# Kernel tuning notes

Measured on AMD Instinct MI355X. Metric: run time of the kernel, lower is better.

## Reference

```python
import jax, jax.numpy as jnp
import numpy as np

N = 12500      # nodes
E = 200000     # edges (avg degree 16)
IN = 32        # inp_dim
OUT = 32       # out_dim
ATTN = 32      # attn_rel_emb_dim
R = 200        # num_rels
NB = 50        # num_bases


def setup_inputs() -> dict:
    key = jax.random.key(0)
    ks = jax.random.split(key, 10)
    node_feat = jax.random.normal(ks[0], (N, IN), jnp.float32)
    total_edge = jax.random.randint(ks[1], (2, E), 0, N)
    total_target_relation = jax.random.normal(ks[2], (E, ATTN), jnp.float32)
    total_relation_embed = jax.random.normal(ks[3], (E, ATTN), jnp.float32)
    total_relation = jax.random.randint(ks[4], (E,), 0, R)
    # learned parameters (xavier-ish scale)
    weight = jax.random.normal(ks[5], (NB, IN, OUT), jnp.float32) * 0.1
    w_comp = jax.random.normal(ks[6], (R, NB), jnp.float32) * 0.1
    self_loop_weight = jax.random.normal(ks[7], (IN, OUT), jnp.float32) * 0.1
    A_w = jax.random.normal(ks[8], (IN, 2 * IN + 2 * ATTN), jnp.float32) * 0.1
    A_b = jnp.zeros((IN,), jnp.float32)
    B_w = jax.random.normal(ks[9], (1, IN), jnp.float32) * 0.1
    B_b = jnp.zeros((1,), jnp.float32)
    return {
        'node_feat': node_feat,
        'total_target_relation': total_target_relation,
        'total_relation_embed': total_relation_embed,
        'weight': weight,
        'w_comp': w_comp,
        'self_loop_weight': self_loop_weight,
        'A_w': A_w,
        'A_b': A_b,
        'B_w': B_w,
        'B_b': B_b,
        'total_edge': total_edge,
        'total_relation': total_relation,
    }


def reference(node_feat, total_target_relation, total_relation_embed,
              weight, w_comp, self_loop_weight, A_w, A_b, B_w, B_b,
              total_edge, total_relation):
    # basis decomposition: per-relation weight [R, IN, OUT]
    rel_w = jnp.einsum('rb,bio->rio', w_comp, weight)
    src = node_feat[total_edge[0]]            # [E, IN]
    tgt = node_feat[total_edge[1]]            # [E, IN]
    # per-edge relation-specific transform (bmm in torch)
    msg = jnp.einsum('ei,eio->eo', src, rel_w[total_relation])  # [E, OUT]
    curr = tgt @ self_loop_weight             # [E, OUT]
    # attention MLP: sigmoid(B(relu(A(concat))))
    e = jnp.concatenate([src, tgt, total_relation_embed, total_target_relation], axis=1)
    h = jax.nn.relu(e @ A_w.T + A_b)
    a = jax.nn.sigmoid(h @ B_w.T + B_b)       # [E, 1]
    curr = curr + msg * a
    # gnn_spmm(e2n_sp, curr): scatter-add edge messages to target nodes
    out = jax.ops.segment_sum(curr, total_edge[1], num_segments=node_feat.shape[0])
    return out  # [N, OUT]
```

## Files before the change

kernel.cpp:

```cpp
#include <hip/hip_runtime.h>

#define N_NODES 12500
#define N_EDGES 200000
#define DIM 32
#define N_REL 200
#define N_BASES 50

#define OUT_ELEMS   (N_NODES * DIM)
#define ZERO_BLOCKS ((OUT_ELEMS + 1023) / 1024)

#define AWBF_OFF  (N_REL * 1024 * 2)
#define SLWT_OFF  (AWBF_OFF + 32 * 128 * 2)

typedef __attribute__((ext_vector_type(8))) short short8;
typedef __attribute__((ext_vector_type(4))) float f32x4;
typedef __attribute__((ext_vector_type(4))) unsigned short us4;

__device__ __forceinline__ unsigned short f2bf(float x) {
    union { float f; unsigned u; } v; v.f = x;
    unsigned r = (v.u + 0x7FFFu + ((v.u >> 16) & 1u)) >> 16;
    return (unsigned short)r;
}

__device__ __forceinline__ short8 cvt8(float4 a, float4 b) {
    short8 r;
    r[0] = (short)f2bf(a.x); r[1] = (short)f2bf(a.y);
    r[2] = (short)f2bf(a.z); r[3] = (short)f2bf(a.w);
    r[4] = (short)f2bf(b.x); r[5] = (short)f2bf(b.y);
    r[6] = (short)f2bf(b.z); r[7] = (short)f2bf(b.w);
    return r;
}

#define MFMA(A, B, C) __builtin_amdgcn_mfma_f32_16x16x32_bf16(A, B, C, 0, 0, 0)

__global__ __launch_bounds__(256) void prep_kernel(
    const float* __restrict__ weight,
    const float* __restrict__ w_comp,
    const float* __restrict__ Aw,
    const float* __restrict__ slw,
    unsigned short* __restrict__ relw_bf,
    unsigned short* __restrict__ aw_bf,
    unsigned short* __restrict__ slwT_bf,
    float* __restrict__ out)
{
    int b = blockIdx.x, tid = threadIdx.x;
    if (b < N_REL) {
        __shared__ float wc[N_BASES];
        if (tid < N_BASES) wc[tid] = w_comp[b * N_BASES + tid];
        __syncthreads();
        const float* wp = weight + tid * 4;
        float4 acc = make_float4(0.f, 0.f, 0.f, 0.f);
        #pragma unroll 10
        for (int bb = 0; bb < N_BASES; bb++) {
            float4 w = *(const float4*)(wp + bb * 1024);
            float c = wc[bb];
            acc.x = fmaf(c, w.x, acc.x); acc.y = fmaf(c, w.y, acc.y);
            acc.z = fmaf(c, w.z, acc.z); acc.w = fmaf(c, w.w, acc.w);
        }
        us4 o;
        o[0] = f2bf(acc.x); o[1] = f2bf(acc.y);
        o[2] = f2bf(acc.z); o[3] = f2bf(acc.w);
        *(us4*)(relw_bf + b * 1024 + tid * 4) = o;
    } else if (b < N_REL + ZERO_BLOCKS) {
        int base = (b - N_REL) * 1024 + tid * 4;
        if (base + 3 < OUT_ELEMS)
            *(float4*)(out + base) = make_float4(0.f, 0.f, 0.f, 0.f);
        else
            for (int k = 0; k < 4; k++)
                if (base + k < OUT_ELEMS) out[base + k] = 0.f;
    } else {
        for (int x = tid; x < 32 * 128; x += 256) aw_bf[x] = f2bf(Aw[x]);
        for (int x = tid; x < 32 * 32; x += 256) {
            int i = x >> 5, j = x & 31;
            slwT_bf[j * 32 + i] = f2bf(slw[x]);
        }
    }
}

__global__ __launch_bounds__(256) void edge_kernel(
    const float* __restrict__ node_feat,
    const float* __restrict__ ttr,
    const float* __restrict__ tre,
    const float* __restrict__ Ab,
    const float* __restrict__ Bw,
    const float* __restrict__ Bb,
    const int*  __restrict__ edge0,
    const int*  __restrict__ edge1,
    const int*  __restrict__ rel,
    const unsigned short* __restrict__ relw_bf,
    const unsigned short* __restrict__ aw_bf,
    const unsigned short* __restrict__ slwT_bf,
    float* __restrict__ out)
{
    __shared__ float msgL[4 * 16 * 36];

    int tid  = threadIdx.x;
    int wave = tid >> 6;
    int lane = tid & 63;
    int m = lane & 15;
    int q = lane >> 4;
    int base = blockIdx.x * 64 + wave * 16;

    int s_ld = 0, t_ld = 0, r_ld = 0;
    if (lane < 16) {
        int eid = base + lane;
        int s = edge0[eid]; s_ld = s < 0 ? 0 : (s >= N_NODES ? N_NODES - 1 : s);
        int t = edge1[eid]; t_ld = t < 0 ? 0 : (t >= N_NODES ? N_NODES - 1 : t);
        int r = rel[eid];   r_ld = r < 0 ? 0 : (r >= N_REL   ? N_REL   - 1 : r);
    }
    int s_m = __shfl(s_ld, m, 64);
    int t_m = __shfl(t_ld, m, 64);
    int eid_m = base + m;

    const float* sp = node_feat + s_m * DIM + q * 8;
    float4 sv0 = *(const float4*)sp, sv1 = *(const float4*)(sp + 4);
    const float* tp = node_feat + t_m * DIM + q * 8;
    float4 tv0 = *(const float4*)tp, tv1 = *(const float4*)(tp + 4);
    const float* rp = tre + eid_m * DIM + q * 8;
    float4 rv0 = *(const float4*)rp, rv1 = *(const float4*)(rp + 4);
    const float* qp = ttr + eid_m * DIM + q * 8;
    float4 qv0 = *(const float4*)qp, qv1 = *(const float4*)(qp + 4);

    short8 fsrc = cvt8(sv0, sv1);
    short8 ftgt = cvt8(tv0, tv1);
    short8 fre  = cvt8(rv0, rv1);
    short8 ftr  = cvt8(qv0, qv1);

    short8 bA[4][2], bS[2];
    #pragma unroll
    for (int hh = 0; hh < 2; hh++) {
        #pragma unroll
        for (int c = 0; c < 4; c++)
            bA[c][hh] = *(const short8*)(aw_bf + (16 * hh + m) * 128 + 32 * c + 8 * q);
        bS[hh] = *(const short8*)(slwT_bf + (16 * hh + m) * 32 + 8 * q);
    }

    float ab0 = Ab[m], ab1 = Ab[16 + m];
    f32x4 hacc0 = {ab0, ab0, ab0, ab0};
    f32x4 hacc1 = {ab1, ab1, ab1, ab1};
    f32x4 cacc0 = {0.f, 0.f, 0.f, 0.f};
    f32x4 cacc1 = {0.f, 0.f, 0.f, 0.f};

    hacc0 = MFMA(fsrc, bA[0][0], hacc0);  hacc1 = MFMA(fsrc, bA[0][1], hacc1);
    hacc0 = MFMA(ftgt, bA[1][0], hacc0);  hacc1 = MFMA(ftgt, bA[1][1], hacc1);
    hacc0 = MFMA(fre,  bA[2][0], hacc0);  hacc1 = MFMA(fre,  bA[2][1], hacc1);
    hacc0 = MFMA(ftr,  bA[3][0], hacc0);  hacc1 = MFMA(ftr,  bA[3][1], hacc1);
    cacc0 = MFMA(ftgt, bS[0], cacc0);     cacc1 = MFMA(ftgt, bS[1], cacc1);

    int e_loc = lane >> 2;
    int cq    = lane & 3;
    int r_e = __shfl(r_ld, e_loc, 64);
    const unsigned short* rwb = relw_bf + r_e * 1024 + cq * 8;
    float sf[8] = {sv0.x, sv0.y, sv0.z, sv0.w, sv1.x, sv1.y, sv1.z, sv1.w};
    float msg[8] = {0.f, 0.f, 0.f, 0.f, 0.f, 0.f, 0.f, 0.f};
    #pragma unroll
    for (int k = 0; k < 32; k++) {
        float s_k = __shfl(sf[k & 7], e_loc + 16 * (k >> 3), 64);
        union { short8 s; unsigned u[4]; } W;
        W.s = *(const short8*)(rwb + k * 32);
        #pragma unroll
        for (int p = 0; p < 4; p++) {
            float lo = __uint_as_float(W.u[p] << 16);
            float hi = __uint_as_float(W.u[p] & 0xffff0000u);
            msg[2 * p]     = fmaf(s_k, lo, msg[2 * p]);
            msg[2 * p + 1] = fmaf(s_k, hi, msg[2 * p + 1]);
        }
    }

    float* ml = msgL + wave * (16 * 36);
    *(float4*)(ml + e_loc * 36 + cq * 8)     = make_float4(msg[0], msg[1], msg[2], msg[3]);
    *(float4*)(ml + e_loc * 36 + cq * 8 + 4) = make_float4(msg[4], msg[5], msg[6], msg[7]);

    float bw0 = Bw[m], bw1 = Bw[16 + m], Bb0 = Bb[0];
    float av[4];
    #pragma unroll
    for (int v = 0; v < 4; v++) {
        float p = fmaxf(hacc0[v], 0.f) * bw0 + fmaxf(hacc1[v], 0.f) * bw1;
        p += __shfl_xor(p, 1, 16);
        p += __shfl_xor(p, 2, 16);
        p += __shfl_xor(p, 4, 16);
        p += __shfl_xor(p, 8, 16);
        av[v] = 1.f / (1.f + __expf(-(p + Bb0)));
    }
    #pragma unroll
    for (int v = 0; v < 4; v++) {
        int row = 4 * q + v;
        int tv = __shfl(t_ld, row, 64);
        float m0 = ml[row * 36 + m];
        float m1 = ml[row * 36 + 16 + m];
        atomicAdd(&out[tv * DIM + m],      cacc0[v] + m0 * av[v]);
        atomicAdd(&out[tv * DIM + 16 + m], cacc1[v] + m1 * av[v]);
    }
}

extern "C" void kernel_launch(void* const* d_in, const int* in_sizes, int n_in,
                              void* d_out, int out_size, void* d_ws, size_t ws_size,
                              hipStream_t stream) {
    const float* node_feat = (const float*)d_in[0];
    const float* ttr       = (const float*)d_in[1];
    const float* tre       = (const float*)d_in[2];
    const float* weight    = (const float*)d_in[3];
    const float* w_comp    = (const float*)d_in[4];
    const float* slw       = (const float*)d_in[5];
    const float* Aw        = (const float*)d_in[6];
    const float* Ab        = (const float*)d_in[7];
    const float* Bw        = (const float*)d_in[8];
    const float* Bb        = (const float*)d_in[9];
    const int*  total_edge = (const int*)d_in[10];
    const int*  rel        = (const int*)d_in[11];
    const int*  edge0 = total_edge;
    const int*  edge1 = total_edge + N_EDGES;

    unsigned short* relw_bf = (unsigned short*)d_ws;
    unsigned short* aw_bf   = (unsigned short*)((char*)d_ws + AWBF_OFF);
    unsigned short* slwT_bf = (unsigned short*)((char*)d_ws + SLWT_OFF);
    float* out = (float*)d_out;

    prep_kernel<<<N_REL + ZERO_BLOCKS + 1, 256, 0, stream>>>(
        weight, w_comp, Aw, slw, relw_bf, aw_bf, slwT_bf, out);

    edge_kernel<<<N_EDGES / 64, 256, 0, stream>>>(
        node_feat, ttr, tre, Ab, Bw, Bb,
        edge0, edge1, rel, relw_bf, aw_bf, slwT_bf, out);
}
```

Baseline: 154.8 us.

## Bucket edges by relation and compute per-edge messages with MFMA

Adds histogram, scan and scatter kernels that group edges by relation into 16-aligned padded buckets. Each wave of 16 edges then shares one relation matrix, so the message transform becomes two bf16 MFMAs instead of a shuffle-and-FMA loop with per-edge weight gathers. The relation weights are stored transposed to fit the MFMA B-operand layout. In exchange it adds three extra kernel launches, atomic counting and scattering, and padding slots that are masked out. Gathers of the edge features now go through an index that no longer follows the original edge order.

```diff
diff --git a/kernel.cpp b/kernel.cpp
--- a/kernel.cpp
+++ b/kernel.cpp
@@ -9,12 +9,21 @@
 #define OUT_ELEMS   (N_NODES * DIM)
 #define ZERO_BLOCKS ((OUT_ELEMS + 1023) / 1024)
 
+#define PE_MAX 203008
+#define INIT_BLOCKS ((PE_MAX + 1023) / 1024)
+
 #define AWBF_OFF  (N_REL * 1024 * 2)
 #define SLWT_OFF  (AWBF_OFF + 32 * 128 * 2)
+#define CNT_OFF   (SLWT_OFF + 32 * 32 * 2)
+#define CUR_OFF   (CNT_OFF + N_REL * 4)
+#define OFF_OFF   (CUR_OFF + N_REL * 4)
+#define SPAD_OFF  (OFF_OFF + N_REL * 4)
+#define TPAD_OFF  (SPAD_OFF + PE_MAX * 4)
+#define EPAD_OFF  (TPAD_OFF + PE_MAX * 4)
+#define RPAD_OFF  (EPAD_OFF + PE_MAX * 4)
 
 typedef __attribute__((ext_vector_type(8))) short short8;
 typedef __attribute__((ext_vector_type(4))) float f32x4;
-typedef __attribute__((ext_vector_type(4))) unsigned short us4;
 
 __device__ __forceinline__ unsigned short f2bf(float x) {
     union { float f; unsigned u; } v; v.f = x;
@@ -38,9 +47,15 @@
     const float* __restrict__ w_comp,
     const float* __restrict__ Aw,
     const float* __restrict__ slw,
-    unsigned short* __restrict__ relw_bf,
+    unsigned short* __restrict__ relwT_bf,
     unsigned short* __restrict__ aw_bf,
     unsigned short* __restrict__ slwT_bf,
+    int* __restrict__ counts,
+    int* __restrict__ cursors,
+    int* __restrict__ spad,
+    int* __restrict__ tpad,
+    int* __restrict__ epad,
+    int* __restrict__ rpad,
     float* __restrict__ out)
 {
     int b = blockIdx.x, tid = threadIdx.x;
@@ -57,10 +72,13 @@
             acc.x = fmaf(c, w.x, acc.x); acc.y = fmaf(c, w.y, acc.y);
             acc.z = fmaf(c, w.z, acc.z); acc.w = fmaf(c, w.w, acc.w);
         }
-        us4 o;
-        o[0] = f2bf(acc.x); o[1] = f2bf(acc.y);
-        o[2] = f2bf(acc.z); o[3] = f2bf(acc.w);
-        *(us4*)(relw_bf + b * 1024 + tid * 4) = o;
+        int i  = tid >> 3;
+        int o0 = (tid * 4) & 31;
+        unsigned short* dst = relwT_bf + b * 1024 + i;
+        dst[(o0 + 0) * 32] = f2bf(acc.x);
+        dst[(o0 + 1) * 32] = f2bf(acc.y);
+        dst[(o0 + 2) * 32] = f2bf(acc.z);
+        dst[(o0 + 3) * 32] = f2bf(acc.w);
     } else if (b < N_REL + ZERO_BLOCKS) {
         int base = (b - N_REL) * 1024 + tid * 4;
         if (base + 3 < OUT_ELEMS)
@@ -68,13 +86,63 @@
         else
             for (int k = 0; k < 4; k++)
                 if (base + k < OUT_ELEMS) out[base + k] = 0.f;
-    } else {
+    } else if (b == N_REL + ZERO_BLOCKS) {
         for (int x = tid; x < 32 * 128; x += 256) aw_bf[x] = f2bf(Aw[x]);
         for (int x = tid; x < 32 * 32; x += 256) {
             int i = x >> 5, j = x & 31;
             slwT_bf[j * 32 + i] = f2bf(slw[x]);
         }
-    }
+        for (int x = tid; x < N_REL; x += 256) { counts[x] = 0; cursors[x] = 0; }
+    } else {
+        int base = (b - (N_REL + ZERO_BLOCKS + 1)) * 1024 + tid * 4;
+        #pragma unroll
+        for (int k = 0; k < 4; k++) {
+            int j = base + k;
+            if (j < PE_MAX) { spad[j] = 0; tpad[j] = -1; epad[j] = 0; rpad[j] = 0; }
+        }
+    }
+}
+
+__global__ __launch_bounds__(256) void hist_kernel(
+    const int* __restrict__ rel, int* __restrict__ counts)
+{
+    int e = blockIdx.x * 256 + threadIdx.x;
+    if (e < N_EDGES) {
+        int r = rel[e]; r = r < 0 ? 0 : (r >= N_REL ? N_REL - 1 : r);
+        atomicAdd(&counts[r], 1);
+    }
+}
+
+__global__ __launch_bounds__(256) void scan_kernel(
+    const int* __restrict__ counts, int* __restrict__ offsets)
+{
+    __shared__ int c[N_REL];
+    int tid = threadIdx.x;
+    for (int x = tid; x < N_REL; x += 256) c[x] = counts[x];
+    __syncthreads();
+    if (tid == 0) {
+        int run = 0;
+        for (int r = 0; r < N_REL; r++) {
+            offsets[r] = run;
+            run += (c[r] + 15) & ~15;
+        }
+    }
+}
+
+__global__ __launch_bounds__(256) void scatter_kernel(
+    const int* __restrict__ edge0, const int* __restrict__ edge1,
+    const int* __restrict__ rel,
+    const int* __restrict__ offsets, int* __restrict__ cursors,
+    int* __restrict__ spad, int* __restrict__ tpad,
+    int* __restrict__ epad, int* __restrict__ rpad)
+{
+    int e = blockIdx.x * 256 + threadIdx.x;
+    if (e >= N_EDGES) return;
+    int r = rel[e];   r = r < 0 ? 0 : (r >= N_REL   ? N_REL   - 1 : r);
+    int s = edge0[e]; s = s < 0 ? 0 : (s >= N_NODES ? N_NODES - 1 : s);
+    int t = edge1[e]; t = t < 0 ? 0 : (t >= N_NODES ? N_NODES - 1 : t);
+    int pos = offsets[r] + atomicAdd(&cursors[r], 1);
+    spad[pos] = s; tpad[pos] = t; epad[pos] = e; rpad[pos] = r;
 }
 
 __global__ __launch_bounds__(256) void edge_kernel(
@@ -84,16 +152,15 @@
     const float* __restrict__ Ab,
     const float* __restrict__ Bw,
     const float* __restrict__ Bb,
-    const int*  __restrict__ edge0,
-    const int*  __restrict__ edge1,
-    const int*  __restrict__ rel,
-    const unsigned short* __restrict__ relw_bf,
+    const int*  __restrict__ spad,
+    const int*  __restrict__ tpad,
+    const int*  __restrict__ epad,
+    const int*  __restrict__ rpad,
+    const unsigned short* __restrict__ relwT_bf,
     const unsigned short* __restrict__ aw_bf,
     const unsigned short* __restrict__ slwT_bf,
     float* __restrict__ out)
 {
-    __shared__ float msgL[4 * 16 * 36];
-
     int tid  = threadIdx.x;
     int wave = tid >> 6;
     int lane = tid & 63;
@@ -101,24 +168,26 @@
     int q = lane >> 4;
     int base = blockIdx.x * 64 + wave * 16;
 
-    int s_ld = 0, t_ld = 0, r_ld = 0;
+    int s_ld = 0, t_ld = -1, e_ld = 0;
     if (lane < 16) {
-        int eid = base + lane;
-        int s = edge0[eid]; s_ld = s < 0 ? 0 : (s >= N_NODES ? N_NODES - 1 : s);
-        int t = edge1[eid]; t_ld = t < 0 ? 0 : (t >= N_NODES ? N_NODES - 1 : t);
-        int r = rel[eid];   r_ld = r < 0 ? 0 : (r >= N_REL   ? N_REL   - 1 : r);
-    }
+        s_ld = spad[base + lane];
+        t_ld = tpad[base + lane];
+        e_ld = epad[base + lane];
+    }
+    int r_w = rpad[base];
+
     int s_m = __shfl(s_ld, m, 64);
     int t_m = __shfl(t_ld, m, 64);
-    int eid_m = base + m;
+    int e_m = __shfl(e_ld, m, 64);
+    int t_mc = t_m < 0 ? 0 : t_m;
 
     const float* sp = node_feat + s_m * DIM + q * 8;
     float4 sv0 = *(const float4*)sp, sv1 = *(const float4*)(sp + 4);
-    const float* tp = node_feat + t_m * DIM + q * 8;
+    const float* tp = node_feat + t_mc * DIM + q * 8;
     float4 tv0 = *(const float4*)tp, tv1 = *(const float4*)(tp + 4);
-    const float* rp = tre + eid_m * DIM + q * 8;
+    const float* rp = tre + e_m * DIM + q * 8;
     float4 rv0 = *(const float4*)rp, rv1 = *(const float4*)(rp + 4);
-    const float* qp = ttr + eid_m * DIM + q * 8;
+    const float* qp = ttr + e_m * DIM + q * 8;
     float4 qv0 = *(const float4*)qp, qv1 = *(const float4*)(qp + 4);
 
     short8 fsrc = cvt8(sv0, sv1);
@@ -126,13 +195,14 @@
     short8 fre  = cvt8(rv0, rv1);
     short8 ftr  = cvt8(qv0, qv1);
 
-    short8 bA[4][2], bS[2];
+    short8 bA[4][2], bS[2], bM[2];
     #pragma unroll
     for (int hh = 0; hh < 2; hh++) {
         #pragma unroll
         for (int c = 0; c < 4; c++)
             bA[c][hh] = *(const short8*)(aw_bf + (16 * hh + m) * 128 + 32 * c + 8 * q);
         bS[hh] = *(const short8*)(slwT_bf + (16 * hh + m) * 32 + 8 * q);
+        bM[hh] = *(const short8*)(relwT_bf + r_w * 1024 + (16 * hh + m) * 32 + 8 * q);
     }
 
     float ab0 = Ab[m], ab1 = Ab[16 + m];
@@ -140,36 +210,15 @@
     f32x4 hacc1 = {ab1, ab1, ab1, ab1};
     f32x4 cacc0 = {0.f, 0.f, 0.f, 0.f};
     f32x4 cacc1 = {0.f, 0.f, 0.f, 0.f};
+    f32x4 macc0 = {0.f, 0.f, 0.f, 0.f};
+    f32x4 macc1 = {0.f, 0.f, 0.f, 0.f};
 
     hacc0 = MFMA(fsrc, bA[0][0], hacc0);  hacc1 = MFMA(fsrc, bA[0][1], hacc1);
     hacc0 = MFMA(ftgt, bA[1][0], hacc0);  hacc1 = MFMA(ftgt, bA[1][1], hacc1);
     hacc0 = MFMA(fre,  bA[2][0], hacc0);  hacc1 = MFMA(fre,  bA[2][1], hacc1);
     hacc0 = MFMA(ftr,  bA[3][0], hacc0);  hacc1 = MFMA(ftr,  bA[3][1], hacc1);
     cacc0 = MFMA(ftgt, bS[0], cacc0);     cacc1 = MFMA(ftgt, bS[1], cacc1);
-
-    int e_loc = lane >> 2;
-    int cq    = lane & 3;
-    int r_e = __shfl(r_ld, e_loc, 64);
-    const unsigned short* rwb = relw_bf + r_e * 1024 + cq * 8;
-    float sf[8] = {sv0.x, sv0.y, sv0.z, sv0.w, sv1.x, sv1.y, sv1.z, sv1.w};
-    float msg[8] = {0.f, 0.f, 0.f, 0.f, 0.f, 0.f, 0.f, 0.f};
-    #pragma unroll
-    for (int k = 0; k < 32; k++) {
-        float s_k = __shfl(sf[k & 7], e_loc + 16 * (k >> 3), 64);
-        union { short8 s; unsigned u[4]; } W;
-        W.s = *(const short8*)(rwb + k * 32);
-        #pragma unroll
-        for (int p = 0; p < 4; p++) {
-            float lo = __uint_as_float(W.u[p] << 16);
-            float hi = __uint_as_float(W.u[p] & 0xffff0000u);
-            msg[2 * p]     = fmaf(s_k, lo, msg[2 * p]);
-            msg[2 * p + 1] = fmaf(s_k, hi, msg[2 * p + 1]);
-        }
-    }
-
-    float* ml = msgL + wave * (16 * 36);
-    *(float4*)(ml + e_loc * 36 + cq * 8)     = make_float4(msg[0], msg[1], msg[2], msg[3]);
-    *(float4*)(ml + e_loc * 36 + cq * 8 + 4) = make_float4(msg[4], msg[5], msg[6], msg[7]);
+    macc0 = MFMA(fsrc, bM[0], macc0);     macc1 = MFMA(fsrc, bM[1], macc1);
 
     float bw0 = Bw[m], bw1 = Bw[16 + m], Bb0 = Bb[0];
     float av[4];
@@ -186,10 +235,10 @@
     for (int v = 0; v < 4; v++) {
         int row = 4 * q + v;
         int tv = __shfl(t_ld, row, 64);
-        float m0 = ml[row * 36 + m];
-        float m1 = ml[row * 36 + 16 + m];
-        atomicAdd(&out[tv * DIM + m],      cacc0[v] + m0 * av[v]);
-        atomicAdd(&out[tv * DIM + 16 + m], cacc1[v] + m1 * av[v]);
+        if (tv >= 0) {
+            atomicAdd(&out[tv * DIM + m],      cacc0[v] + macc0[v] * av[v]);
+            atomicAdd(&out[tv * DIM + 16 + m], cacc1[v] + macc1[v] * av[v]);
+        }
     }
 }
 
@@ -211,15 +260,31 @@
     const int*  edge0 = total_edge;
     const int*  edge1 = total_edge + N_EDGES;
 
-    unsigned short* relw_bf = (unsigned short*)d_ws;
-    unsigned short* aw_bf   = (unsigned short*)((char*)d_ws + AWBF_OFF);
-    unsigned short* slwT_bf = (unsigned short*)((char*)d_ws + SLWT_OFF);
+    char* ws = (char*)d_ws;
+    unsigned short* relwT_bf = (unsigned short*)ws;
+    unsigned short* aw_bf    = (unsigned short*)(ws + AWBF_OFF);
+    unsigned short* slwT_bf  = (unsigned short*)(ws + SLWT_OFF);
+    int* counts  = (int*)(ws + CNT_OFF);
+    int* cursors = (int*)(ws + CUR_OFF);
+    int* offsets = (int*)(ws + OFF_OFF);
+    int* spad    = (int*)(ws + SPAD_OFF);
+    int* tpad    = (int*)(ws + TPAD_OFF);
+    int* epad    = (int*)(ws + EPAD_OFF);
+    int* rpad    = (int*)(ws + RPAD_OFF);
     float* out = (float*)d_out;
 
-    prep_kernel<<<N_REL + ZERO_BLOCKS + 1, 256, 0, stream>>>(
-        weight, w_comp, Aw, slw, relw_bf, aw_bf, slwT_bf, out);
-
-    edge_kernel<<<N_EDGES / 64, 256, 0, stream>>>(
+    prep_kernel<<<N_REL + ZERO_BLOCKS + 1 + INIT_BLOCKS, 256, 0, stream>>>(
+        weight, w_comp, Aw, slw, relwT_bf, aw_bf, slwT_bf,
+        counts, cursors, spad, tpad, epad, rpad, out);
+
+    hist_kernel<<<(N_EDGES + 255) / 256, 256, 0, stream>>>(rel, counts);
+
+    scan_kernel<<<1, 256, 0, stream>>>(counts, offsets);
+
+    scatter_kernel<<<(N_EDGES + 255) / 256, 256, 0, stream>>>(
+        edge0, edge1, rel, offsets, cursors, spad, tpad, epad, rpad);
+
+    edge_kernel<<<PE_MAX / 64, 256, 0, stream>>>(
         node_feat, ttr, tre, Ab, Bw, Bb,
-        edge0, edge1, rel, relw_bf, aw_bf, slwT_bf, out);
-}
+        spad, tpad, epad, rpad, relwT_bf, aw_bf, slwT_bf, out);
+}
```

After: 395.1 us. 2.55x slower.
